# Kernel tuning notes

Hardware: AMD Instinct MI355X
Metric: run time of the kernel (lower is better)

Reference implementation:

```python
import jax, jax.numpy as jnp
import numpy as np

B, T, D = 2, 128, 1024
H, R, Dk, Dv = 8, 8, 64, 64


def setup_inputs() -> dict:
    key = jax.random.key(0)
    ks = jax.random.split(key, 11)
    w = lambda k, shp: jax.random.normal(k, shp, dtype=jnp.float32) * 0.02
    return {
        "hidden_states": jax.random.normal(ks[0], (B, T, D), dtype=jnp.float32),
        "Wq": w(ks[1], (D, H * Dk)),
        "Wk": w(ks[2], (D, H * Dk)),
        "Wv": w(ks[3], (D, H * Dv)),
        "Wb": w(ks[4], (D, H * R)),
        "Wtg": w(ks[5], (D, H * R)),
        "mode_logits": jax.random.normal(ks[6], (H, R), dtype=jnp.float32) * 0.1,
        "log_decay": jax.random.normal(ks[7], (H, R), dtype=jnp.float32) * 0.1,
        "omega_log_scale": jax.random.normal(ks[8], (H, R), dtype=jnp.float32) * 0.1,
        "Wg": w(ks[9], (D, H * Dv)),
        "Wo": w(ks[10], (H * Dv, D)),
    }


def _forward(x, Wq, Wk, Wv, Wb, Wtg, mode_logits, log_decay, omega_log_scale, Wg, Wo):
    b, t, _ = x.shape
    # projections
    q = (x @ Wq).reshape(b, t, H, Dk)
    k = (x @ Wk).reshape(b, t, H, Dk)
    v = (x @ Wv).reshape(b, t, H, Dv)
    beta = jax.nn.sigmoid((x @ Wb).reshape(b, t, H, R))
    tg = jax.nn.sigmoid((x @ Wtg).reshape(b, t, H, R))
    # spectral mode parameters
    pair_idx = jnp.arange(0, Dk, 2, dtype=jnp.float32)
    inv_freq = 1.0 / (10000.0 ** (pair_idx / Dk))            # [Dk/2]
    omega = jnp.exp(omega_log_scale)[..., None] * inv_freq    # [H,R,Dk/2]
    omega_full = jnp.repeat(omega, 2, axis=-1)                # [H,R,Dk] (repeat_interleave)
    cos_w = jnp.cos(omega_full)[None, :, :, None, :]          # [1,H,R,1,Dk]
    sin_w = jnp.sin(omega_full)[None, :, :, None, :]
    rho = jnp.exp(-jax.nn.softplus(log_decay))                # [H,R]
    mode_w = jax.nn.softmax(mode_logits, axis=-1)             # [H,R]

    # time-major for scan
    qT = jnp.moveaxis(q, 1, 0)
    kT = jnp.moveaxis(k, 1, 0)
    vT = jnp.moveaxis(v, 1, 0)
    betaT = jnp.moveaxis(beta, 1, 0)
    tgT = jnp.moveaxis(tg, 1, 0)

    def step(carry, xs):
        sr, si = carry                      # [B,H,R,Dv,Dk] each
        q_t, k_t, v_t, b_t, g_t = xs
        decay = (g_t * rho)[..., None, None]            # [B,H,R,1,1]
        rot_r = decay * (cos_w * sr - sin_w * si)
        rot_i = decay * (sin_w * sr + cos_w * si)
        pred = jnp.einsum('bhrvk,bhk->bhrv', rot_r, k_t)
        err = v_t[:, :, None, :] - pred                  # [B,H,R,Dv]
        write = err[..., None] * k_t[:, :, None, None, :]
        sr_new = rot_r + b_t[..., None, None] * write
        read = jnp.einsum('bhrvk,bhk->bhrv', sr_new, q_t)
        y = jnp.einsum('bhrv,hr->bhv', read, mode_w)     # [B,H,Dv]
        return (sr_new, rot_i), y

    s0 = jnp.zeros((b, H, R, Dv, Dk), dtype=x.dtype)
    _, ys = jax.lax.scan(step, (s0, s0), (qT, kT, vT, betaT, tgT))
    o = jnp.moveaxis(ys, 0, 1)                           # [B,T,H,Dv]
    gate = jax.nn.sigmoid((x @ Wg).reshape(b, t, H, Dv))
    o = (o * gate).reshape(b, t, H * Dv)
    return o @ Wo


def reference(hidden_states, Wq, Wk, Wv, Wb, Wtg, mode_logits, log_decay,
              omega_log_scale, Wg, Wo):
    return _forward(hidden_states, Wq, Wk, Wv, Wb, Wtg, mode_logits,
                    log_decay, omega_log_scale, Wg, Wo)
```

## Files before the change

kernel.cpp:

```cpp
#include <hip/hip_runtime.h>
#include <math.h>

#define T_ 128
#define NPROJ 2176
#define CH 32

typedef __attribute__((ext_vector_type(8))) short short8;
typedef __attribute__((ext_vector_type(4))) float float4v;
typedef __attribute__((ext_vector_type(2))) float float2v;

__device__ __forceinline__ ushort f2bf(float x) {
    unsigned u = __float_as_uint(x);
    u += 0x7FFF + ((u >> 16) & 1);
    return (ushort)(u >> 16);
}

__global__ __launch_bounds__(256) void prep_kernel(
    const float* __restrict__ x,
    const float* __restrict__ Wq, const float* __restrict__ Wk,
    const float* __restrict__ Wv, const float* __restrict__ Wb,
    const float* __restrict__ Wtg, const float* __restrict__ Wg,
    const float* __restrict__ Wo,
    const float* __restrict__ mode_logits, const float* __restrict__ log_decay,
    const float* __restrict__ ols,
    float* __restrict__ cosw, float* __restrict__ sinw,
    float* __restrict__ rho, float* __restrict__ modew,
    ushort* __restrict__ xb, ushort* __restrict__ wtb, ushort* __restrict__ wotb,
    float* __restrict__ Acomb)
{
    __shared__ ushort tile[64][68];
    const int blk = blockIdx.x, tid = threadIdx.x;
    if (blk < 16) {
        int idx = blk * 256 + tid;
        if (idx >= 64 * 64) return;
        int t = idx >> 6;
        int k = idx & 63;
        int h = t >> 3;
        if (k == 0) {
            float ld = log_decay[t];
            rho[t] = 1.0f / (1.0f + expf(ld));
            float m = -1e30f;
            for (int i = 0; i < 8; i++) m = fmaxf(m, mode_logits[h * 8 + i]);
            float sum = 0.0f;
            for (int i = 0; i < 8; i++) sum += expf(mode_logits[h * 8 + i] - m);
            modew[t] = expf(mode_logits[t] - m) / sum;
        }
        float osc = expf(ols[t]);
        int p = k >> 1;
        float invf = expf(-((float)(2 * p) / 64.0f) * logf(10000.0f));
        float w = osc * invf;
        cosw[idx] = cosf(w);
        sinw[idx] = sinf(w);
        return;
    }
    if (blk < 80) {
        int base = (blk - 16) * 4096 + tid * 16;
        float4 f0 = *(const float4*)&x[base];
        float4 f1 = *(const float4*)&x[base + 4];
        float4 f2 = *(const float4*)&x[base + 8];
        float4 f3 = *(const float4*)&x[base + 12];
        short8 o0, o1;
        o0[0]=f2bf(f0.x); o0[1]=f2bf(f0.y); o0[2]=f2bf(f0.z); o0[3]=f2bf(f0.w);
        o0[4]=f2bf(f1.x); o0[5]=f2bf(f1.y); o0[6]=f2bf(f1.z); o0[7]=f2bf(f1.w);
        o1[0]=f2bf(f2.x); o1[1]=f2bf(f2.y); o1[2]=f2bf(f2.z); o1[3]=f2bf(f2.w);
        o1[4]=f2bf(f3.x); o1[5]=f2bf(f3.y); o1[6]=f2bf(f3.z); o1[7]=f2bf(f3.w);
        *(short8*)&xb[base] = o0;
        *(short8*)&xb[base + 8] = o1;
        return;
    }
    if (blk >= 752) {
        int base = (blk - 752) * 4096 + tid * 16;
        float4 z = make_float4(0.f, 0.f, 0.f, 0.f);
        *(float4*)&Acomb[base] = z;
        *(float4*)&Acomb[base + 4] = z;
        *(float4*)&Acomb[base + 8] = z;
        *(float4*)&Acomb[base + 12] = z;
        return;
    }
    const float* src; int ld, c0, n0, k0, ldd; ushort* dst;
    if (blk < 624) {
        int b3 = blk - 80; int nt = b3 >> 4, kt = b3 & 15;
        n0 = nt * 64; k0 = kt * 64;
        if (n0 < 512)       { src = Wq;  c0 = n0;        ld = 512; }
        else if (n0 < 1024) { src = Wk;  c0 = n0 - 512;  ld = 512; }
        else if (n0 < 1536) { src = Wv;  c0 = n0 - 1024; ld = 512; }
        else if (n0 < 1600) { src = Wb;  c0 = n0 - 1536; ld = 64;  }
        else if (n0 < 1664) { src = Wtg; c0 = n0 - 1600; ld = 64;  }
        else                { src = Wg;  c0 = n0 - 1664; ld = 512; }
        dst = wtb; ldd = 1024;
    } else {
        int b4 = blk - 624; int nt = b4 >> 3, kt = b4 & 7;
        n0 = nt * 64; k0 = kt * 64;
        src = Wo; c0 = n0; ld = 1024; dst = wotb; ldd = 512;
    }
    #pragma unroll
    for (int rep = 0; rep < 4; rep++) {
        int k = rep * 16 + (tid >> 4);
        int nc = (tid & 15) * 4;
        float4 f = *(const float4*)&src[(size_t)(k0 + k) * ld + c0 + nc];
        tile[nc + 0][k] = f2bf(f.x);
        tile[nc + 1][k] = f2bf(f.y);
        tile[nc + 2][k] = f2bf(f.z);
        tile[nc + 3][k] = f2bf(f.w);
    }
    __syncthreads();
    #pragma unroll
    for (int rep = 0; rep < 4; rep++) {
        int n = rep * 16 + (tid >> 4);
        int kc = (tid & 15) * 4;
        uint2 u = *(const uint2*)&tile[n][kc];
        *(uint2*)&dst[(size_t)(n0 + n) * ldd + k0 + kc] = u;
    }
}

__global__ __launch_bounds__(256, 2) void proj_mfma(const ushort* __restrict__ Ab,
        const ushort* __restrict__ BTb, float* __restrict__ proj)
{
    __shared__ ushort sA[2][64][40];
    __shared__ ushort sB[2][64][40];
    const int n0 = blockIdx.x * 64, m0 = blockIdx.y * 64;
    const int tid = threadIdx.x;
    const int lane = tid & 63, w = tid >> 6;
    const int wm = w & 1, wn = w >> 1;
    const int l16 = lane & 15, quad = lane >> 4;
    const int srow = tid >> 2, skq = (tid & 3) * 8;
    const ushort* Ag = Ab + (size_t)(m0 + srow) * 1024 + skq;
    const ushort* Bg = BTb + (size_t)(n0 + srow) * 1024 + skq;
    short8 ra = *(const short8*)Ag;
    short8 rb = *(const short8*)Bg;
    float4v acc00 = {0,0,0,0}, acc01 = {0,0,0,0}, acc10 = {0,0,0,0}, acc11 = {0,0,0,0};
    for (int kt = 0; kt < 32; kt++) {
        const int cb = kt & 1;
        *(short8*)&sA[cb][srow][skq] = ra;
        *(short8*)&sB[cb][srow][skq] = rb;
        __syncthreads();
        if (kt + 1 < 32) {
            ra = *(const short8*)(Ag + (kt + 1) * 32);
            rb = *(const short8*)(Bg + (kt + 1) * 32);
        }
        short8 a0 = *(const short8*)&sA[cb][wm * 32 + l16][quad * 8];
        short8 a1 = *(const short8*)&sA[cb][wm * 32 + 16 + l16][quad * 8];
        short8 b0 = *(const short8*)&sB[cb][wn * 32 + l16][quad * 8];
        short8 b1 = *(const short8*)&sB[cb][wn * 32 + 16 + l16][quad * 8];
        acc00 = __builtin_amdgcn_mfma_f32_16x16x32_bf16(a0, b0, acc00, 0, 0, 0);
        acc01 = __builtin_amdgcn_mfma_f32_16x16x32_bf16(a0, b1, acc01, 0, 0, 0);
        acc10 = __builtin_amdgcn_mfma_f32_16x16x32_bf16(a1, b0, acc10, 0, 0, 0);
        acc11 = __builtin_amdgcn_mfma_f32_16x16x32_bf16(a1, b1, acc11, 0, 0, 0);
    }
    const bool sig = (n0 >= 1536);
    const int colb = n0 + wn * 32 + l16;
    const int rowb = m0 + wm * 32 + quad * 4;
    #pragma unroll
    for (int r2 = 0; r2 < 4; r2++) {
        float v00 = acc00[r2], v01 = acc01[r2], v10 = acc10[r2], v11 = acc11[r2];
        if (sig) {
            v00 = 1.0f / (1.0f + expf(-v00));
            v01 = 1.0f / (1.0f + expf(-v01));
            v10 = 1.0f / (1.0f + expf(-v10));
            v11 = 1.0f / (1.0f + expf(-v11));
        }
        proj[(size_t)(rowb + r2) * NPROJ + colb] = v00;
        proj[(size_t)(rowb + r2) * NPROJ + colb + 16] = v01;
        proj[(size_t)(rowb + 16 + r2) * NPROJ + colb] = v10;
        proj[(size_t)(rowb + 16 + r2) * NPROJ + colb + 16] = v11;
    }
}

template<int CTRL>
__device__ __forceinline__ float dpp_add(float x) {
    int xi = __float_as_int(x);
    int yi = __builtin_amdgcn_update_dpp(xi, xi, CTRL, 0xF, 0xF, false);
    return x + __int_as_float(yi);
}

__global__ __launch_bounds__(256, 2) void scan_kernel(const float* __restrict__ proj,
        const float* __restrict__ cosw, const float* __restrict__ sinw,
        const float* __restrict__ rho, const float* __restrict__ modew,
        float* __restrict__ Acomb)
{
    __shared__ float qk[2][CH][128];
    __shared__ float vbuf[2][CH][16];
    __shared__ float gbuf[2][CH][16];
    __shared__ float sc4[2][CH][4];

    const int bi = blockIdx.x;
    const int s  = bi & 3;
    const int hr = (bi >> 2) & 63;
    const int b  = bi >> 8;
    const int h = hr >> 3, r = hr & 7;
    const int tid = threadIdx.x;
    const int vl = tid >> 4;
    const int kl = tid & 15;

    float2v cw0, cw1, sw0, sw1;
    cw0.x = cosw[hr * 64 + kl * 4 + 0]; cw0.y = cosw[hr * 64 + kl * 4 + 1];
    cw1.x = cosw[hr * 64 + kl * 4 + 2]; cw1.y = cosw[hr * 64 + kl * 4 + 3];
    sw0.x = sinw[hr * 64 + kl * 4 + 0]; sw0.y = sinw[hr * 64 + kl * 4 + 1];
    sw1.x = sinw[hr * 64 + kl * 4 + 2]; sw1.y = sinw[hr * 64 + kl * 4 + 3];
    const float rho_hr = rho[hr];
    const float mw = modew[hr];
    float2v sr0 = {0,0}, sr1 = {0,0}, si0 = {0,0}, si1 = {0,0};

    const float* pb = proj + (size_t)b * T_ * NPROJ;
    const int qbase = h * 64;
    const int kbase = 512 + h * 64;
    const int vbase = 1024 + h * 64 + s * 16;
    const int gbase = 1664 + h * 64 + s * 16;
    const int boff  = 1536 + h * 8 + r;
    const int goff  = 1600 + h * 8 + r;

    auto stage = [&](int t0, int nb) {
        #pragma unroll
        for (int rep = 0; rep < 4; rep++) {
            int idx = rep * 256 + tid;
            int t = idx >> 5, sub = idx & 31;
            const float* row = pb + (size_t)(t0 + t) * NPROJ;
            float4 val = *(const float4*)(row + (sub < 16 ? qbase + sub * 4
                                                          : kbase + (sub - 16) * 4));
            *(float4*)&qk[nb][t][sub * 4] = val;
        }
        if (tid < 128) {
            int t = tid >> 2, sub = tid & 3;
            *(float4*)&vbuf[nb][t][sub * 4] =
                *(const float4*)(pb + (size_t)(t0 + t) * NPROJ + vbase + sub * 4);
        } else {
            int t = (tid - 128) >> 2, sub = tid & 3;
            *(float4*)&gbuf[nb][t][sub * 4] =
                *(const float4*)(pb + (size_t)(t0 + t) * NPROJ + gbase + sub * 4);
        }
        if (tid < CH)            sc4[nb][tid][0]      = pb[(size_t)(t0 + tid) * NPROJ + boff];
        else if (tid < 2 * CH)   sc4[nb][tid - CH][1] = pb[(size_t)(t0 + tid - CH) * NPROJ + goff];
    };

    stage(0, 0);
    __syncthreads();

    float* dst = Acomb + ((size_t)b * 128) * 512 + h * 64 + s * 16 + vl;

    for (int c = 0; c < T_ / CH; c++) {
        const int cb = c & 1;
        {
            int t = tid >> 3, j = tid & 7;
            float4 ka = *(const float4*)&qk[cb][t][64 + j * 8];
            float4 kb4 = *(const float4*)&qk[cb][t][64 + j * 8 + 4];
            float4 qa = *(const float4*)&qk[cb][t][j * 8];
            float4 qb4 = *(const float4*)&qk[cb][t][j * 8 + 4];
            float p = ka.x * qa.x + ka.y * qa.y + ka.z * qa.z + ka.w * qa.w
                    + kb4.x * qb4.x + kb4.y * qb4.y + kb4.z * qb4.z + kb4.w * qb4.w;
            p = dpp_add<0xB1>(p);
            p = dpp_add<0x4E>(p);
            p = dpp_add<0x141>(p);
            if (j == 0) sc4[cb][t][2] = p;
        }
        __syncthreads();
        if (c + 1 < T_ / CH) stage((c + 1) * CH, (c + 1) & 1);

        #pragma unroll 4
        for (int t = 0; t < CH; t++) {
            float4 kf = *(const float4*)&qk[cb][t][64 + kl * 4];
            float4 qf = *(const float4*)&qk[cb][t][kl * 4];
            float4 sv = *(const float4*)&sc4[cb][t][0];
            const float vv = vbuf[cb][t][vl];
            const float gate = gbuf[cb][t][vl];

            const float decay = sv.y * rho_hr;
            float2v k0; k0.x = kf.x; k0.y = kf.y;
            float2v k1; k1.x = kf.z; k1.y = kf.w;
            float2v q0; q0.x = qf.x; q0.y = qf.y;
            float2v q1; q1.x = qf.z; q1.y = qf.w;

            float2v t1 = cw0 * sr0 - sw0 * si0;
            float2v u1 = sw0 * sr0 + cw0 * si0;
            float2v t2 = cw1 * sr1 - sw1 * si1;
            float2v u2 = sw1 * sr1 + cw1 * si1;
            float2v d2; d2.x = decay; d2.y = decay;
            float2v rr0 = d2 * t1, rr1 = d2 * t2;
            si0 = d2 * u1; si1 = d2 * u2;

            float2v pk2 = rr0 * k0 + rr1 * k1;
            float2v pq2 = rr0 * q0 + rr1 * q1;
            float pk = pk2.x + pk2.y;
            float pq = pq2.x + pq2.y;
            pk = dpp_add<0xB1>(pk);  pq = dpp_add<0xB1>(pq);
            pk = dpp_add<0x4E>(pk);  pq = dpp_add<0x4E>(pq);
            pk = dpp_add<0x141>(pk); pq = dpp_add<0x141>(pq);
            pk = dpp_add<0x140>(pk); pq = dpp_add<0x140>(pq);

            const float sc = sv.x * (vv - pk);
            float2v sc2; sc2.x = sc; sc2.y = sc;
            sr0 = rr0 + sc2 * k0;
            sr1 = rr1 + sc2 * k1;
            const float rp = pq + sc * sv.z;
            if (kl == 0) atomicAdd(dst + (size_t)(c * CH + t) * 512, mw * rp * gate);
        }
        __syncthreads();
    }
}

__global__ __launch_bounds__(256, 2) void out_mfma(const float* __restrict__ Af,
        const ushort* __restrict__ BTb, float* __restrict__ C)
{
    __shared__ ushort sA[2][64][40];
    __shared__ ushort sB[2][64][40];
    const int n0 = blockIdx.x * 64, m0 = blockIdx.y * 64;
    const int tid = threadIdx.x;
    const int lane = tid & 63, w = tid >> 6;
    const int wm = w & 1, wn = w >> 1;
    const int l16 = lane & 15, quad = lane >> 4;
    const int srow = tid >> 2, skq = (tid & 3) * 8;
    const float* Ag = Af + (size_t)(m0 + srow) * 512 + skq;
    const ushort* Bg = BTb + (size_t)(n0 + srow) * 512 + skq;
    float4 fa0 = *(const float4*)Ag;
    float4 fa1 = *(const float4*)(Ag + 4);
    short8 rb = *(const short8*)Bg;
    float4v acc00 = {0,0,0,0}, acc01 = {0,0,0,0}, acc10 = {0,0,0,0}, acc11 = {0,0,0,0};
    for (int kt = 0; kt < 16; kt++) {
        const int cb = kt & 1;
        short8 ra;
        ra[0]=f2bf(fa0.x); ra[1]=f2bf(fa0.y); ra[2]=f2bf(fa0.z); ra[3]=f2bf(fa0.w);
        ra[4]=f2bf(fa1.x); ra[5]=f2bf(fa1.y); ra[6]=f2bf(fa1.z); ra[7]=f2bf(fa1.w);
        *(short8*)&sA[cb][srow][skq] = ra;
        *(short8*)&sB[cb][srow][skq] = rb;
        __syncthreads();
        if (kt + 1 < 16) {
            fa0 = *(const float4*)(Ag + (kt + 1) * 32);
            fa1 = *(const float4*)(Ag + (kt + 1) * 32 + 4);
            rb = *(const short8*)(Bg + (kt + 1) * 32);
        }
        short8 a0 = *(const short8*)&sA[cb][wm * 32 + l16][quad * 8];
        short8 a1 = *(const short8*)&sA[cb][wm * 32 + 16 + l16][quad * 8];
        short8 b0 = *(const short8*)&sB[cb][wn * 32 + l16][quad * 8];
        short8 b1 = *(const short8*)&sB[cb][wn * 32 + 16 + l16][quad * 8];
        acc00 = __builtin_amdgcn_mfma_f32_16x16x32_bf16(a0, b0, acc00, 0, 0, 0);
        acc01 = __builtin_amdgcn_mfma_f32_16x16x32_bf16(a0, b1, acc01, 0, 0, 0);
        acc10 = __builtin_amdgcn_mfma_f32_16x16x32_bf16(a1, b0, acc10, 0, 0, 0);
        acc11 = __builtin_amdgcn_mfma_f32_16x16x32_bf16(a1, b1, acc11, 0, 0, 0);
    }
    const int colb = n0 + wn * 32 + l16;
    const int rowb = m0 + wm * 32 + quad * 4;
    #pragma unroll
    for (int r2 = 0; r2 < 4; r2++) {
        C[(size_t)(rowb + r2) * 1024 + colb] = acc00[r2];
        C[(size_t)(rowb + r2) * 1024 + colb + 16] = acc01[r2];
        C[(size_t)(rowb + 16 + r2) * 1024 + colb] = acc10[r2];
        C[(size_t)(rowb + 16 + r2) * 1024 + colb + 16] = acc11[r2];
    }
}

extern "C" void kernel_launch(void* const* d_in, const int* in_sizes, int n_in,
                              void* d_out, int out_size, void* d_ws, size_t ws_size,
                              hipStream_t stream) {
    const float* x   = (const float*)d_in[0];
    const float* Wq  = (const float*)d_in[1];
    const float* Wk  = (const float*)d_in[2];
    const float* Wv  = (const float*)d_in[3];
    const float* Wb  = (const float*)d_in[4];
    const float* Wtg = (const float*)d_in[5];
    const float* ml  = (const float*)d_in[6];
    const float* ldc = (const float*)d_in[7];
    const float* ols = (const float*)d_in[8];
    const float* Wg  = (const float*)d_in[9];
    const float* Wo  = (const float*)d_in[10];
    float* out = (float*)d_out;

    float* ws = (float*)d_ws;
    float* proj    = ws;
    float* cosw    = proj + 256 * NPROJ;
    float* sinw    = cosw + 4096;
    float* rho     = sinw + 4096;
    float* modew   = rho + 64;
    ushort* xb     = (ushort*)(modew + 64);
    ushort* wotb   = (ushort*)((float*)xb + 131072);
    float*  Acomb  = (float*)wotb + 262144;
    ushort* wtb    = (ushort*)(Acomb + 131072);

    prep_kernel<<<784, 256, 0, stream>>>(x, Wq, Wk, Wv, Wb, Wtg, Wg, Wo,
                                         ml, ldc, ols, cosw, sinw, rho, modew,
                                         xb, wtb, wotb, Acomb);
    proj_mfma<<<dim3(34, 4), 256, 0, stream>>>(xb, wtb, proj);
    scan_kernel<<<512, 256, 0, stream>>>(proj, cosw, sinw, rho, modew, Acomb);
    out_mfma<<<dim3(16, 4), 256, 0, stream>>>(Acomb, wotb, out);
}
```

Baseline: 140.2 us.

## Split scan state across 32 lanes per value row with 512-thread blocks

The scan kernel doubles its block size to 512 threads, so each thread holds 2 state elements instead of 4 (32 lanes per v-row rather than 16). This halves the per-thread serial arithmetic in the recurrence. In exchange, each reduction needs an extra cross-row swizzle step, and the pk/pq reductions are packed into float2 DPP ops. The v and gate buffers are merged into one float2 shared array, and the q·k precompute is re-split to 16 lanes per timestep. The risk is lower occupancy per block and the extra ds_swizzle latency on the serial critical path.

```diff
diff --git a/kernel.cpp b/kernel.cpp
--- a/kernel.cpp
+++ b/kernel.cpp
@@ -13,6 +13,26 @@
     unsigned u = __float_as_uint(x);
     u += 0x7FFF + ((u >> 16) & 1);
     return (ushort)(u >> 16);
+}
+
+template<int CTRL>
+__device__ __forceinline__ float dpp_add(float x) {
+    int xi = __float_as_int(x);
+    int yi = __builtin_amdgcn_update_dpp(xi, xi, CTRL, 0xF, 0xF, false);
+    return x + __int_as_float(yi);
+}
+template<int CTRL>
+__device__ __forceinline__ float2v dpp_add2(float2v x) {
+    int lo = __builtin_amdgcn_update_dpp(__float_as_int(x.x), __float_as_int(x.x), CTRL, 0xF, 0xF, false);
+    int hi = __builtin_amdgcn_update_dpp(__float_as_int(x.y), __float_as_int(x.y), CTRL, 0xF, 0xF, false);
+    float2v o; o.x = __int_as_float(lo); o.y = __int_as_float(hi);
+    return x + o;
+}
+__device__ __forceinline__ float2v swz16_add2(float2v x) {
+    int lo = __builtin_amdgcn_ds_swizzle(__float_as_int(x.x), 0x401F);
+    int hi = __builtin_amdgcn_ds_swizzle(__float_as_int(x.y), 0x401F);
+    float2v o; o.x = __int_as_float(lo); o.y = __int_as_float(hi);
+    return x + o;
 }
 
 __global__ __launch_bounds__(256) void prep_kernel(
@@ -108,8 +128,8 @@
     for (int rep = 0; rep < 4; rep++) {
         int n = rep * 16 + (tid >> 4);
         int kc = (tid & 15) * 4;
-        uint2 u = *(const uint2*)&tile[n][kc];
-        *(uint2*)&dst[(size_t)(n0 + n) * ldd + k0 + kc] = u;
+        uint2 uu = *(const uint2*)&tile[n][kc];
+        *(uint2*)&dst[(size_t)(n0 + n) * ldd + k0 + kc] = uu;
     }
 }
 
@@ -166,21 +186,13 @@
     }
 }
 
-template<int CTRL>
-__device__ __forceinline__ float dpp_add(float x) {
-    int xi = __float_as_int(x);
-    int yi = __builtin_amdgcn_update_dpp(xi, xi, CTRL, 0xF, 0xF, false);
-    return x + __int_as_float(yi);
-}
-
-__global__ __launch_bounds__(256, 2) void scan_kernel(const float* __restrict__ proj,
+__global__ __launch_bounds__(512, 2) void scan_kernel(const float* __restrict__ proj,
         const float* __restrict__ cosw, const float* __restrict__ sinw,
         const float* __restrict__ rho, const float* __restrict__ modew,
         float* __restrict__ Acomb)
 {
     __shared__ float qk[2][CH][128];
-    __shared__ float vbuf[2][CH][16];
-    __shared__ float gbuf[2][CH][16];
+    __shared__ float2 vg[2][CH][16];
     __shared__ float sc4[2][CH][4];
 
     const int bi = blockIdx.x;
@@ -189,17 +201,15 @@
     const int b  = bi >> 8;
     const int h = hr >> 3, r = hr & 7;
     const int tid = threadIdx.x;
-    const int vl = tid >> 4;
-    const int kl = tid & 15;
-
-    float2v cw0, cw1, sw0, sw1;
-    cw0.x = cosw[hr * 64 + kl * 4 + 0]; cw0.y = cosw[hr * 64 + kl * 4 + 1];
-    cw1.x = cosw[hr * 64 + kl * 4 + 2]; cw1.y = cosw[hr * 64 + kl * 4 + 3];
-    sw0.x = sinw[hr * 64 + kl * 4 + 0]; sw0.y = sinw[hr * 64 + kl * 4 + 1];
-    sw1.x = sinw[hr * 64 + kl * 4 + 2]; sw1.y = sinw[hr * 64 + kl * 4 + 3];
+    const int vl = tid >> 5;
+    const int kl = tid & 31;
+
+    float2v cw, sw;
+    cw.x = cosw[hr * 64 + kl * 2];  cw.y = cosw[hr * 64 + kl * 2 + 1];
+    sw.x = sinw[hr * 64 + kl * 2];  sw.y = sinw[hr * 64 + kl * 2 + 1];
     const float rho_hr = rho[hr];
     const float mw = modew[hr];
-    float2v sr0 = {0,0}, sr1 = {0,0}, si0 = {0,0}, si1 = {0,0};
+    float2v sr = {0,0}, si = {0,0};
 
     const float* pb = proj + (size_t)b * T_ * NPROJ;
     const int qbase = h * 64;
@@ -211,22 +221,18 @@
 
     auto stage = [&](int t0, int nb) {
         #pragma unroll
-        for (int rep = 0; rep < 4; rep++) {
-            int idx = rep * 256 + tid;
+        for (int rep = 0; rep < 2; rep++) {
+            int idx = rep * 512 + tid;
             int t = idx >> 5, sub = idx & 31;
             const float* row = pb + (size_t)(t0 + t) * NPROJ;
             float4 val = *(const float4*)(row + (sub < 16 ? qbase + sub * 4
                                                           : kbase + (sub - 16) * 4));
             *(float4*)&qk[nb][t][sub * 4] = val;
         }
-        if (tid < 128) {
-            int t = tid >> 2, sub = tid & 3;
-            *(float4*)&vbuf[nb][t][sub * 4] =
-                *(const float4*)(pb + (size_t)(t0 + t) * NPROJ + vbase + sub * 4);
-        } else {
-            int t = (tid - 128) >> 2, sub = tid & 3;
-            *(float4*)&gbuf[nb][t][sub * 4] =
-                *(const float4*)(pb + (size_t)(t0 + t) * NPROJ + gbase + sub * 4);
+        {
+            int t = tid >> 4, v2 = tid & 15;
+            const float* row = pb + (size_t)(t0 + t) * NPROJ;
+            vg[nb][t][v2] = make_float2(row[vbase + v2], row[gbase + v2]);
         }
         if (tid < CH)            sc4[nb][tid][0]      = pb[(size_t)(t0 + tid) * NPROJ + boff];
         else if (tid < 2 * CH)   sc4[nb][tid - CH][1] = pb[(size_t)(t0 + tid - CH) * NPROJ + goff];
@@ -240,16 +246,14 @@
     for (int c = 0; c < T_ / CH; c++) {
         const int cb = c & 1;
         {
-            int t = tid >> 3, j = tid & 7;
-            float4 ka = *(const float4*)&qk[cb][t][64 + j * 8];
-            float4 kb4 = *(const float4*)&qk[cb][t][64 + j * 8 + 4];
-            float4 qa = *(const float4*)&qk[cb][t][j * 8];
-            float4 qb4 = *(const float4*)&qk[cb][t][j * 8 + 4];
-            float p = ka.x * qa.x + ka.y * qa.y + ka.z * qa.z + ka.w * qa.w
-                    + kb4.x * qb4.x + kb4.y * qb4.y + kb4.z * qb4.z + kb4.w * qb4.w;
+            int t = tid >> 4, j = tid & 15;
+            float4 ka = *(const float4*)&qk[cb][t][64 + j * 4];
+            float4 qa = *(const float4*)&qk[cb][t][j * 4];
+            float p = ka.x * qa.x + ka.y * qa.y + ka.z * qa.z + ka.w * qa.w;
             p = dpp_add<0xB1>(p);
             p = dpp_add<0x4E>(p);
             p = dpp_add<0x141>(p);
+            p = dpp_add<0x140>(p);
             if (j == 0) sc4[cb][t][2] = p;
         }
         __syncthreads();
@@ -257,41 +261,32 @@
 
         #pragma unroll 4
         for (int t = 0; t < CH; t++) {
-            float4 kf = *(const float4*)&qk[cb][t][64 + kl * 4];
-            float4 qf = *(const float4*)&qk[cb][t][kl * 4];
+            float2v kf = *(const float2v*)&qk[cb][t][64 + kl * 2];
+            float2v qf = *(const float2v*)&qk[cb][t][kl * 2];
             float4 sv = *(const float4*)&sc4[cb][t][0];
-            const float vv = vbuf[cb][t][vl];
-            const float gate = gbuf[cb][t][vl];
+            float2 vgv = vg[cb][t][vl];
 
             const float decay = sv.y * rho_hr;
-            float2v k0; k0.x = kf.x; k0.y = kf.y;
-            float2v k1; k1.x = kf.z; k1.y = kf.w;
-            float2v q0; q0.x = qf.x; q0.y = qf.y;
-            float2v q1; q1.x = qf.z; q1.y = qf.w;
-
-            float2v t1 = cw0 * sr0 - sw0 * si0;
-            float2v u1 = sw0 * sr0 + cw0 * si0;
-            float2v t2 = cw1 * sr1 - sw1 * si1;
-            float2v u2 = sw1 * sr1 + cw1 * si1;
+            float2v t1 = cw * sr - sw * si;
+            float2v u1 = sw * sr + cw * si;
             float2v d2; d2.x = decay; d2.y = decay;
-            float2v rr0 = d2 * t1, rr1 = d2 * t2;
-            si0 = d2 * u1; si1 = d2 * u2;
-
-            float2v pk2 = rr0 * k0 + rr1 * k1;
-            float2v pq2 = rr0 * q0 + rr1 * q1;
-            float pk = pk2.x + pk2.y;
-            float pq = pq2.x + pq2.y;
-            pk = dpp_add<0xB1>(pk);  pq = dpp_add<0xB1>(pq);
-            pk = dpp_add<0x4E>(pk);  pq = dpp_add<0x4E>(pq);
-            pk = dpp_add<0x141>(pk); pq = dpp_add<0x141>(pq);
-            pk = dpp_add<0x140>(pk); pq = dpp_add<0x140>(pq);
-
-            const float sc = sv.x * (vv - pk);
+            float2v rr = d2 * t1;
+            si = d2 * u1;
+
+            float2v pk2 = rr * kf;
+            float2v pq2 = rr * qf;
+            float2v pp; pp.x = pk2.x + pk2.y; pp.y = pq2.x + pq2.y;
+            pp = dpp_add2<0xB1>(pp);
+            pp = dpp_add2<0x4E>(pp);
+            pp = dpp_add2<0x141>(pp);
+            pp = dpp_add2<0x140>(pp);
+            pp = swz16_add2(pp);
+
+            const float sc = sv.x * (vgv.x - pp.x);
             float2v sc2; sc2.x = sc; sc2.y = sc;
-            sr0 = rr0 + sc2 * k0;
-            sr1 = rr1 + sc2 * k1;
-            const float rp = pq + sc * sv.z;
-            if (kl == 0) atomicAdd(dst + (size_t)(c * CH + t) * 512, mw * rp * gate);
+            sr = rr + sc2 * kf;
+            const float rp = pp.y + sc * sv.z;
+            if (kl == 0) atomicAdd(dst + (size_t)(c * CH + t) * 512, mw * rp * vgv.y);
         }
         __syncthreads();
     }
@@ -378,6 +373,6 @@
                                          ml, ldc, ols, cosw, sinw, rho, modew,
                                          xb, wtb, wotb, Acomb);
     proj_mfma<<<dim3(34, 4), 256, 0, stream>>>(xb, wtb, proj);
-    scan_kernel<<<512, 256, 0, stream>>>(proj, cosw, sinw, rho, modew, Acomb);
+    scan_kernel<<<512, 512, 0, stream>>>(proj, cosw, sinw, rho, modew, Acomb);
     out_mfma<<<dim3(16, 4), 256, 0, stream>>>(Acomb, wotb, out);
 }
```

After: 151.2 us. 7.8% more time.
